# Kernel optimization log

Hardware: AMD Instinct MI355X
Metric: run time of the kernel (lower is better)

## Reference

```python
import jax, jax.numpy as jnp
import numpy as np

N = 100000
IN_C = 256
OUT_C = 256
E = 500000


def gcn_conv(x, W, b, edges):
    """PyG GCNConv: add self-loops, symmetric D^-1/2 (A+I) D^-1/2 normalization,
    then scatter-add of transformed source features into targets, plus bias."""
    n = x.shape[0]
    loop = jnp.arange(n, dtype=edges.dtype)
    row = jnp.concatenate([edges[0], loop])  # source
    col = jnp.concatenate([edges[1], loop])  # target
    deg = jax.ops.segment_sum(jnp.ones_like(col, dtype=x.dtype), col, num_segments=n)
    dis = jax.lax.rsqrt(deg)  # deg >= 1 after self-loops
    norm = dis[row] * dis[col]  # [E+n]
    h = x @ W  # [n, out]
    msg = h[row] * norm[:, None]  # gather + scale
    return jax.ops.segment_sum(msg, col, num_segments=n) + b


def setup_inputs() -> dict:
    key = jax.random.key(0)
    ks = jax.random.split(key, 24)
    x = jax.random.normal(ks[0], (N, IN_C), dtype=jnp.float32)
    edges00 = jax.random.randint(ks[1], (2, E), 0, N, dtype=jnp.int32)
    edges01 = jax.random.randint(ks[2], (2, E), 0, N, dtype=jnp.int32)
    edges10 = jax.random.randint(ks[3], (2, E), 0, N, dtype=jnp.int32)
    edges11 = jax.random.randint(ks[4], (2, E), 0, N, dtype=jnp.int32)
    t0 = (jax.random.uniform(ks[5], (N,)) > 0.5).astype(jnp.float32)
    t1 = 1.0 - t0
    scale = 1.0 / np.sqrt(IN_C)
    W1 = jax.random.normal(ks[6], (IN_C, OUT_C), dtype=jnp.float32) * scale
    W2 = jax.random.normal(ks[7], (IN_C, OUT_C), dtype=jnp.float32) * scale
    W3 = jax.random.normal(ks[8], (IN_C, OUT_C), dtype=jnp.float32) * scale
    W4 = jax.random.normal(ks[9], (IN_C, OUT_C), dtype=jnp.float32) * scale
    b1 = jnp.zeros((OUT_C,), jnp.float32)
    b2 = jnp.zeros((OUT_C,), jnp.float32)
    b3 = jnp.zeros((OUT_C,), jnp.float32)
    b4 = jnp.zeros((OUT_C,), jnp.float32)
    p0 = jax.random.normal(ks[10], (OUT_C,), dtype=jnp.float32)
    p1 = jax.random.normal(ks[11], (OUT_C,), dtype=jnp.float32)
    p2 = jax.random.normal(ks[12], (OUT_C,), dtype=jnp.float32)
    p3 = jax.random.normal(ks[13], (OUT_C,), dtype=jnp.float32)
    p4 = jax.random.normal(ks[14], (OUT_C,), dtype=jnp.float32)
    p5 = jax.random.normal(ks[15], (OUT_C,), dtype=jnp.float32)
    return dict(x=x, edges00=edges00, edges01=edges01, edges10=edges10, edges11=edges11,
                type0_idx=t0, type1_idx=t1,
                W1=W1, b1=b1, W2=W2, b2=b2, W3=W3, b3=b3, W4=W4, b4=b4,
                p0=p0, p1=p1, p2=p2, p3=p3, p4=p4, p5=p5)


def reference(x, edges00, edges01, edges10, edges11, type0_idx, type1_idx,
              W1, b1, W2, b2, W3, b3, W4, b4, p0, p1, p2, p3, p4, p5):
    # x0/x1: first feature column masked by node type, broadcast over out channels
    x0c = type0_idx * x[:, 0]  # [N]
    x1c = type1_idx * x[:, 0]
    x00 = gcn_conv(x, W1, b1, edges00)
    x01 = gcn_conv(x, W2, b2, edges01)
    x10 = gcn_conv(x, W3, b3, edges10)
    x11 = gcn_conv(x, W4, b4, edges11)
    out = (x0c[:, None] * p0 + x1c[:, None] * p1
           + x00 * p2 + x01 * p3 + x10 * p4 + x11 * p5)
    return out
```

## Files before the change

### kernel.cpp

```cpp
#include <hip/hip_runtime.h>


#define PCAP 24

typedef __bf16 v8bf __attribute__((ext_vector_type(8)));
typedef float v4f __attribute__((ext_vector_type(4)));

__device__ __forceinline__ unsigned short f2bf(float f) {
  unsigned u = __float_as_uint(f);
  u += 0x7fffu + ((u >> 16) & 1u);
  return (unsigned short)(u >> 16);
}
__device__ __forceinline__ float bf2f(unsigned short s) {
  return __uint_as_float(((unsigned)s) << 16);
}
__device__ __forceinline__ void async_ld16(const void* g, void* l) {
  __builtin_amdgcn_global_load_lds((__attribute__((address_space(1))) void*)g,
                                   (__attribute__((address_space(3))) void*)l,
                                   16, 0, 0);
}

__global__ void lc_fill(const int* __restrict__ e0, const int* __restrict__ e1,
                        const int* __restrict__ e2, const int* __restrict__ e3,
                        int* __restrict__ cursor, unsigned* __restrict__ payload,
                        int N, int E) {
  int e = blockIdx.x * 256 + threadIdx.x;
  if (e >= E) return;
  int k = blockIdx.y;
  const int* ed = (k == 0) ? e0 : (k == 1) ? e1 : (k == 2) ? e2 : e3;
  int src = ed[e], col = ed[E + e];
  int idx = k * N + col;
  int pos = atomicAdd(&cursor[idx], 1);
  if (pos < PCAP) payload[(size_t)idx * PCAP + pos] = (unsigned)src;
}

__global__ void lc_pack(unsigned* __restrict__ payload, const int* __restrict__ deg,
                        int N) {
  int i = blockIdx.x * 256 + threadIdx.x;
  if (i >= N * PCAP) return;
  int k = blockIdx.y;
  int col = i / PCAP, slot = i - col * PCAP;
  int list = k * N + col;
  int cnt = deg[list];
  if (cnt > PCAP) cnt = PCAP;
  if (slot >= cnt) return;
  size_t pidx = (size_t)list * PCAP + slot;
  unsigned src = payload[pidx];
  float ds = rsqrtf((float)(deg[(size_t)k * N + src] + 1));
  unsigned q = (unsigned)(ds * 32767.0f + 0.5f);
  payload[pidx] = (q << 17) | src;
}

__global__ void lc_prep(const float* __restrict__ W1, const float* __restrict__ W2,
                        const float* __restrict__ W3, const float* __restrict__ W4,
                        const float* __restrict__ b1, const float* __restrict__ b2,
                        const float* __restrict__ b3, const float* __restrict__ b4,
                        const float* __restrict__ p2, const float* __restrict__ p3,
                        const float* __restrict__ p4, const float* __restrict__ p5,
                        unsigned short* __restrict__ Wt, float* __restrict__ biasc) {
  __shared__ float tile[256][33];
  int k = blockIdx.y, co0 = blockIdx.x * 32;
  int t = threadIdx.x;
  const float* W = (k == 0) ? W1 : (k == 1) ? W2 : (k == 2) ? W3 : W4;
  const float* p = (k == 0) ? p2 : (k == 1) ? p3 : (k == 2) ? p4 : p5;

  if (blockIdx.x == 0 && k == 0) {
    int c = t;
    biasc[c] = b1[c] * p2[c] + b2[c] * p3[c] + b3[c] * p4[c] + b4[c] * p5[c];
  }

  int coL = t & 31, kkB = t >> 5;
#pragma unroll 4
  for (int pass = 0; pass < 32; ++pass) {
    int kk = pass * 8 + kkB;
    tile[kk][coL] = W[kk * 256 + co0 + coL];
  }
  __syncthreads();

  int co = t >> 3, seg0 = t & 7;
  float pv = p[co0 + co];
#pragma unroll
  for (int i = 0; i < 4; ++i) {
    int s = seg0 + 8 * i;
    ushort4 lo, hi;
    int kk = s * 8;
    lo.x = f2bf(tile[kk + 0][co] * pv); lo.y = f2bf(tile[kk + 1][co] * pv);
    lo.z = f2bf(tile[kk + 2][co] * pv); lo.w = f2bf(tile[kk + 3][co] * pv);
    hi.x = f2bf(tile[kk + 4][co] * pv); hi.y = f2bf(tile[kk + 5][co] * pv);
    hi.z = f2bf(tile[kk + 6][co] * pv); hi.w = f2bf(tile[kk + 7][co] * pv);
    unsigned short* dst = Wt + (size_t)(co0 + co) * 1024 + k * 256 + kk;
    *(ushort4*)dst = lo;
    *(ushort4*)(dst + 4) = hi;
  }
}

__global__ void lc_cvt(const float4* __restrict__ x4, ushort4* __restrict__ xb4,
                       const float* __restrict__ t0, const float* __restrict__ t1,
                       float* __restrict__ m0, float* __restrict__ m1, int n4) {
  int i = blockIdx.x * 256 + threadIdx.x;
  if (i >= n4) return;
  float4 v = x4[i];
  ushort4 r;
  r.x = f2bf(v.x); r.y = f2bf(v.y); r.z = f2bf(v.z); r.w = f2bf(v.w);
  xb4[i] = r;
  if ((i & 63) == 0) {
    int n = i >> 6;
    float xc = v.x;
    m0[n] = t0[n] * xc;
    m1[n] = t1[n] * xc;
  }
}

__global__ __launch_bounds__(256) void lc_aggx(
    const unsigned short* __restrict__ xb, unsigned short* __restrict__ Agg,
    int aggw, int kcount, int kbase, const int* __restrict__ deg,
    const unsigned* __restrict__ payload, int N) {
  int t = threadIdx.x;
  int w = t >> 6, lane = t & 63;
  int n, k, koff;
  if (kcount == 4) { n = blockIdx.x; k = w; koff = k * 256; }
  else { n = blockIdx.x * 4 + w; k = kbase; koff = 0; }
  if (n >= N) return;
  int c = lane * 4;
  int idx = k * N + n;

  int degv = deg[idx];
  float dn = rsqrtf((float)(degv + 1));
  float dns = dn * (1.0f / 32767.0f);
  float s = dn * dn;
  ushort4 hv = *(const ushort4*)&xb[(size_t)n * 256 + c];
  float a0 = bf2f(hv.x) * s, a1 = bf2f(hv.y) * s;
  float a2 = bf2f(hv.z) * s, a3 = bf2f(hv.w) * s;

  size_t start = (size_t)idx * PCAP;
  int cnt = (degv > PCAP) ? PCAP : degv;
  int i = 0;
  for (; i + 4 <= cnt; i += 4) {
    unsigned p0v = payload[start + i];
    unsigned p1v = payload[start + i + 1];
    unsigned p2v = payload[start + i + 2];
    unsigned p3v = payload[start + i + 3];
    unsigned s0 = p0v & 0x1FFFFu, s1 = p1v & 0x1FFFFu;
    unsigned s2 = p2v & 0x1FFFFu, s3 = p3v & 0x1FFFFu;
    ushort4 g0 = *(const ushort4*)&xb[(size_t)s0 * 256 + c];
    ushort4 g1 = *(const ushort4*)&xb[(size_t)s1 * 256 + c];
    ushort4 g2 = *(const ushort4*)&xb[(size_t)s2 * 256 + c];
    ushort4 g3 = *(const ushort4*)&xb[(size_t)s3 * 256 + c];
    float n0 = (float)(p0v >> 17) * dns, n1 = (float)(p1v >> 17) * dns;
    float n2 = (float)(p2v >> 17) * dns, n3 = (float)(p3v >> 17) * dns;
    a0 += bf2f(g0.x) * n0 + bf2f(g1.x) * n1 + bf2f(g2.x) * n2 + bf2f(g3.x) * n3;
    a1 += bf2f(g0.y) * n0 + bf2f(g1.y) * n1 + bf2f(g2.y) * n2 + bf2f(g3.y) * n3;
    a2 += bf2f(g0.z) * n0 + bf2f(g1.z) * n1 + bf2f(g2.z) * n2 + bf2f(g3.z) * n3;
    a3 += bf2f(g0.w) * n0 + bf2f(g1.w) * n1 + bf2f(g2.w) * n2 + bf2f(g3.w) * n3;
  }
  for (; i < cnt; i++) {
    unsigned p0v = payload[start + i];
    unsigned s0 = p0v & 0x1FFFFu;
    ushort4 g0 = *(const ushort4*)&xb[(size_t)s0 * 256 + c];
    float n0 = (float)(p0v >> 17) * dns;
    a0 += bf2f(g0.x) * n0;
    a1 += bf2f(g0.y) * n0;
    a2 += bf2f(g0.z) * n0;
    a3 += bf2f(g0.w) * n0;
  }
  ushort4 r;
  r.x = f2bf(a0); r.y = f2bf(a1); r.z = f2bf(a2); r.w = f2bf(a3);
  *(ushort4*)&Agg[(size_t)n * aggw + koff + c] = r;
}

__global__ __launch_bounds__(512) void lc_gemm(
    const unsigned short* __restrict__ A, int strideA,
    const unsigned short* __restrict__ B, int strideB, int K,
    float* __restrict__ out, int Mrows, int addprev, int doepi,
    const float* __restrict__ m0, const float* __restrict__ m1,
    const float* __restrict__ p0, const float* __restrict__ p1,
    const float* __restrict__ biasc) {
  __shared__ alignas(16) unsigned short As[2][128 * 32];
  __shared__ alignas(16) unsigned short Bs[2][256 * 32];
  int t = threadIdx.x;
  int w = t >> 6, lane = t & 63;
  int wm = w & 1, wn = w >> 1;
  int quad = lane >> 4, l16 = lane & 15;
  int row0 = blockIdx.x * 128;

  v4f acc[4][4];
#pragma unroll
  for (int mt = 0; mt < 4; mt++)
#pragma unroll
    for (int nt = 0; nt < 4; nt++) {
      v4f z = {0.f, 0.f, 0.f, 0.f};
      acc[mt][nt] = z;
    }

  const int ra = t >> 2;
  const int e0 = (t & 3) * 8;
  const int sws = (ra & 3) << 3;
  const unsigned swf = (unsigned)((l16 & 3) << 3);

  int growA = row0 + ra;
  if (growA >= Mrows) growA = Mrows - 1;
  const unsigned short* Ap = A + (size_t)growA * strideA + (e0 ^ sws);
  const unsigned short* Bp0 = B + (size_t)ra * strideB + (e0 ^ sws);
  const unsigned short* Bp1 = B + (size_t)(128 + ra) * strideB + (e0 ^ sws);
  const int lA = ra * 32 + e0;
  const int lB0 = ra * 32 + e0, lB1 = (128 + ra) * 32 + e0;

  async_ld16(Ap, &As[0][lA]);
  async_ld16(Bp0, &Bs[0][lB0]);
  async_ld16(Bp1, &Bs[0][lB1]);
  asm volatile("s_waitcnt vmcnt(0)" ::: "memory");
  __builtin_amdgcn_s_barrier();

  int cur = 0;
  for (int kk = 0; kk < K; kk += 32) {
    if (kk + 32 < K) {
      async_ld16(Ap + kk + 32, &As[cur ^ 1][lA]);
      async_ld16(Bp0 + kk + 32, &Bs[cur ^ 1][lB0]);
      async_ld16(Bp1 + kk + 32, &Bs[cur ^ 1][lB1]);
    }

    v8bf af[4], bfr[4];
    unsigned eq = ((unsigned)(quad * 8)) ^ swf;
#pragma unroll
    for (int mt = 0; mt < 4; mt++) {
      int r = wm * 64 + mt * 16 + l16;
      af[mt] = *(const v8bf*)&As[cur][(unsigned)r * 32 + eq];
    }
#pragma unroll
    for (int nt = 0; nt < 4; nt++) {
      int n = wn * 64 + nt * 16 + l16;
      bfr[nt] = *(const v8bf*)&Bs[cur][(unsigned)n * 32 + eq];
    }
#pragma unroll
    for (int mt = 0; mt < 4; mt++)
#pragma unroll
      for (int nt = 0; nt < 4; nt++)
        acc[mt][nt] =
            __builtin_amdgcn_mfma_f32_16x16x32_bf16(af[mt], bfr[nt], acc[mt][nt], 0, 0, 0);

    asm volatile("s_waitcnt vmcnt(0)" ::: "memory");
    __builtin_amdgcn_s_barrier();
    cur ^= 1;
  }

  float pc0[4], pc1[4], bc[4];
#pragma unroll
  for (int nt = 0; nt < 4; nt++) {
    int gcol = wn * 64 + nt * 16 + l16;
    pc0[nt] = doepi ? p0[gcol] : 0.f;
    pc1[nt] = doepi ? p1[gcol] : 0.f;
    bc[nt] = doepi ? biasc[gcol] : 0.f;
  }
#pragma unroll
  for (int mt = 0; mt < 4; mt++)
#pragma unroll
    for (int r = 0; r < 4; r++) {
      int grow = row0 + wm * 64 + mt * 16 + quad * 4 + r;
      if (grow >= Mrows) continue;
      float m0v = 0.f, m1v = 0.f;
      if (doepi) { m0v = m0[grow]; m1v = m1[grow]; }
#pragma unroll
      for (int nt = 0; nt < 4; nt++) {
        int gcol = wn * 64 + nt * 16 + l16;
        size_t o = (size_t)grow * 256 + gcol;
        float v = acc[mt][nt][r];
        if (addprev) v += out[o];
        if (doepi) v += m0v * pc0[nt] + m1v * pc1[nt] + bc[nt];
        out[o] = v;
      }
    }
}

extern "C" void kernel_launch(void* const* d_in, const int* in_sizes, int n_in,
                              void* d_out, int out_size, void* d_ws, size_t ws_size,
                              hipStream_t stream) {
  const float* x = (const float*)d_in[0];
  const int* e00 = (const int*)d_in[1];
  const int* e01 = (const int*)d_in[2];
  const int* e10 = (const int*)d_in[3];
  const int* e11 = (const int*)d_in[4];
  const float* t0 = (const float*)d_in[5];
  const float* t1 = (const float*)d_in[6];
  const float* W1 = (const float*)d_in[7];
  const float* b1 = (const float*)d_in[8];
  const float* W2 = (const float*)d_in[9];
  const float* b2 = (const float*)d_in[10];
  const float* W3 = (const float*)d_in[11];
  const float* b3 = (const float*)d_in[12];
  const float* W4 = (const float*)d_in[13];
  const float* b4 = (const float*)d_in[14];
  const float* p0 = (const float*)d_in[15];
  const float* p1 = (const float*)d_in[16];
  const float* p2 = (const float*)d_in[17];
  const float* p3 = (const float*)d_in[18];
  const float* p4 = (const float*)d_in[19];
  const float* p5 = (const float*)d_in[20];
  float* out = (float*)d_out;

  int N = in_sizes[0] / 256;
  int E = in_sizes[1] / 2;
  int M4 = 4 * N;

  char* wp = (char*)d_ws;
  auto carve = [&](size_t bytes) {
    void* r = (void*)wp;
    wp += (bytes + 255) & ~(size_t)255;
    return r;
  };
  unsigned short* xb = (unsigned short*)carve((size_t)N * 256 * 2);
  unsigned short* Wt = (unsigned short*)carve((size_t)256 * 1024 * 2);
  int* cursor = (int*)carve((size_t)M4 * 4);
  float* biasc = (float*)carve(256 * 4);
  float* m0 = (float*)carve((size_t)N * 4);
  float* m1 = (float*)carve((size_t)N * 4);
  unsigned* payload = (unsigned*)carve((size_t)M4 * PCAP * 4);
  size_t used = (size_t)(wp - (char*)d_ws);
  size_t remain = (ws_size > used) ? ws_size - used : 0;
  bool fat = remain >= (size_t)N * 1024 * 2;
  unsigned short* Agg = (unsigned short*)wp;

  int gE = (E + 255) / 256;
  int gP = (N * PCAP + 255) / 256;

  hipMemsetAsync(cursor, 0, (size_t)M4 * 4, stream);
  lc_fill<<<dim3(gE, 4), 256, 0, stream>>>(e00, e01, e10, e11, cursor, payload, N, E);
  lc_pack<<<dim3(gP, 4), 256, 0, stream>>>(payload, cursor, N);
  lc_prep<<<dim3(8, 4), 256, 0, stream>>>(W1, W2, W3, W4, b1, b2, b3, b4,
                                          p2, p3, p4, p5, Wt, biasc);
  lc_cvt<<<(N * 64 + 255) / 256, 256, 0, stream>>>((const float4*)x, (ushort4*)xb,
                                                   t0, t1, m0, m1, N * 64);

  int gemm_mb = (N + 127) / 128;
  if (fat) {
    lc_aggx<<<N, 256, 0, stream>>>(xb, Agg, 1024, 4, 0, cursor, payload, N);
    lc_gemm<<<gemm_mb, 512, 0, stream>>>(Agg, 1024, Wt, 1024, 1024, out, N,
                                         0, 1, m0, m1, p0, p1, biasc);
  } else {
    for (int k = 0; k < 4; k++) {
      lc_aggx<<<(N + 3) / 4, 256, 0, stream>>>(xb, Agg, 256, 1, k, cursor,
                                               payload, N);
      lc_gemm<<<gemm_mb, 512, 0, stream>>>(Agg, 256, Wt + k * 256, 1024, 256,
                                           out, N, (k > 0) ? 1 : 0,
                                           (k == 3) ? 1 : 0, m0, m1, p0, p1,
                                           biasc);
    }
  }
}
```

Measured before the change: 700.0 us.

## Fuse payload packing into fill via separate degree histogram; aggregate two nodes per wave

Adds a histogram pass that computes in-degrees first, so the fill kernel can write the packed source-and-normalization word directly and the separate pack pass goes away. The aggregation kernel now has each wave process two destination nodes at once, with predicated, clamped gathers that keep more independent loads in flight. This costs an extra pass over the edge lists and extra memset traffic. Nodes with unequal degrees also issue wasted clamped loads up to the larger count.

```diff
diff --git a/kernel.cpp b/kernel.cpp
--- a/kernel.cpp
+++ b/kernel.cpp
@@ -20,10 +20,21 @@
                                    16, 0, 0);
 }
 
+__global__ void lc_hist(const int* __restrict__ e0, const int* __restrict__ e1,
+                        const int* __restrict__ e2, const int* __restrict__ e3,
+                        int* __restrict__ deg, int N, int E) {
+  int e = blockIdx.x * 256 + threadIdx.x;
+  if (e >= E) return;
+  int k = blockIdx.y;
+  const int* ed = (k == 0) ? e0 : (k == 1) ? e1 : (k == 2) ? e2 : e3;
+  int col = ed[E + e];
+  atomicAdd(&deg[k * N + col], 1);
+}
+
 __global__ void lc_fill(const int* __restrict__ e0, const int* __restrict__ e1,
                         const int* __restrict__ e2, const int* __restrict__ e3,
-                        int* __restrict__ cursor, unsigned* __restrict__ payload,
-                        int N, int E) {
+                        const int* __restrict__ deg, int* __restrict__ cursor,
+                        unsigned* __restrict__ payload, int N, int E) {
   int e = blockIdx.x * 256 + threadIdx.x;
   if (e >= E) return;
   int k = blockIdx.y;
@@ -31,24 +42,11 @@
   int src = ed[e], col = ed[E + e];
   int idx = k * N + col;
   int pos = atomicAdd(&cursor[idx], 1);
-  if (pos < PCAP) payload[(size_t)idx * PCAP + pos] = (unsigned)src;
-}
-
-__global__ void lc_pack(unsigned* __restrict__ payload, const int* __restrict__ deg,
-                        int N) {
-  int i = blockIdx.x * 256 + threadIdx.x;
-  if (i >= N * PCAP) return;
-  int k = blockIdx.y;
-  int col = i / PCAP, slot = i - col * PCAP;
-  int list = k * N + col;
-  int cnt = deg[list];
-  if (cnt > PCAP) cnt = PCAP;
-  if (slot >= cnt) return;
-  size_t pidx = (size_t)list * PCAP + slot;
-  unsigned src = payload[pidx];
-  float ds = rsqrtf((float)(deg[(size_t)k * N + src] + 1));
-  unsigned q = (unsigned)(ds * 32767.0f + 0.5f);
-  payload[pidx] = (q << 17) | src;
+  if (pos < PCAP) {
+    float ds = rsqrtf((float)(deg[(size_t)k * N + src] + 1));
+    unsigned q = (unsigned)(ds * 32767.0f + 0.5f);
+    payload[(size_t)idx * PCAP + pos] = (q << 17) | (unsigned)src;
+  }
 }
 
 __global__ void lc_prep(const float* __restrict__ W1, const float* __restrict__ W2,
@@ -111,61 +109,68 @@
   }
 }
 
+#define GATP(BASE, POS, LIM, CNT, DNS, A0, A1, A2, A3)                  \
+  do {                                                                  \
+    int jj = ((POS) < (CNT)) ? (POS) : (LIM);                           \
+    unsigned pv = payload[(BASE) + jj];                                 \
+    unsigned ss = pv & 0x1FFFFu;                                        \
+    ushort4 gg = *(const ushort4*)&xb[(size_t)ss * 256 + c];            \
+    float nn = ((POS) < (CNT)) ? (float)(pv >> 17) * (DNS) : 0.f;       \
+    A0 += bf2f(gg.x) * nn;                                              \
+    A1 += bf2f(gg.y) * nn;                                              \
+    A2 += bf2f(gg.z) * nn;                                              \
+    A3 += bf2f(gg.w) * nn;                                              \
+  } while (0)
+
 __global__ __launch_bounds__(256) void lc_aggx(
     const unsigned short* __restrict__ xb, unsigned short* __restrict__ Agg,
     int aggw, int kcount, int kbase, const int* __restrict__ deg,
     const unsigned* __restrict__ payload, int N) {
   int t = threadIdx.x;
   int w = t >> 6, lane = t & 63;
-  int n, k, koff;
-  if (kcount == 4) { n = blockIdx.x; k = w; koff = k * 256; }
-  else { n = blockIdx.x * 4 + w; k = kbase; koff = 0; }
-  if (n >= N) return;
+  int n0, k, koff;
+  if (kcount == 4) { n0 = blockIdx.x * 2; k = w; koff = k * 256; }
+  else { n0 = blockIdx.x * 8 + w * 2; k = kbase; koff = 0; }
+  if (n0 >= N) return;
   int c = lane * 4;
-  int idx = k * N + n;
-
-  int degv = deg[idx];
-  float dn = rsqrtf((float)(degv + 1));
-  float dns = dn * (1.0f / 32767.0f);
-  float s = dn * dn;
-  ushort4 hv = *(const ushort4*)&xb[(size_t)n * 256 + c];
-  float a0 = bf2f(hv.x) * s, a1 = bf2f(hv.y) * s;
-  float a2 = bf2f(hv.z) * s, a3 = bf2f(hv.w) * s;
-
-  size_t start = (size_t)idx * PCAP;
-  int cnt = (degv > PCAP) ? PCAP : degv;
-  int i = 0;
-  for (; i + 4 <= cnt; i += 4) {
-    unsigned p0v = payload[start + i];
-    unsigned p1v = payload[start + i + 1];
-    unsigned p2v = payload[start + i + 2];
-    unsigned p3v = payload[start + i + 3];
-    unsigned s0 = p0v & 0x1FFFFu, s1 = p1v & 0x1FFFFu;
-    unsigned s2 = p2v & 0x1FFFFu, s3 = p3v & 0x1FFFFu;
-    ushort4 g0 = *(const ushort4*)&xb[(size_t)s0 * 256 + c];
-    ushort4 g1 = *(const ushort4*)&xb[(size_t)s1 * 256 + c];
-    ushort4 g2 = *(const ushort4*)&xb[(size_t)s2 * 256 + c];
-    ushort4 g3 = *(const ushort4*)&xb[(size_t)s3 * 256 + c];
-    float n0 = (float)(p0v >> 17) * dns, n1 = (float)(p1v >> 17) * dns;
-    float n2 = (float)(p2v >> 17) * dns, n3 = (float)(p3v >> 17) * dns;
-    a0 += bf2f(g0.x) * n0 + bf2f(g1.x) * n1 + bf2f(g2.x) * n2 + bf2f(g3.x) * n3;
-    a1 += bf2f(g0.y) * n0 + bf2f(g1.y) * n1 + bf2f(g2.y) * n2 + bf2f(g3.y) * n3;
-    a2 += bf2f(g0.z) * n0 + bf2f(g1.z) * n1 + bf2f(g2.z) * n2 + bf2f(g3.z) * n3;
-    a3 += bf2f(g0.w) * n0 + bf2f(g1.w) * n1 + bf2f(g2.w) * n2 + bf2f(g3.w) * n3;
-  }
-  for (; i < cnt; i++) {
-    unsigned p0v = payload[start + i];
-    unsigned s0 = p0v & 0x1FFFFu;
-    ushort4 g0 = *(const ushort4*)&xb[(size_t)s0 * 256 + c];
-    float n0 = (float)(p0v >> 17) * dns;
-    a0 += bf2f(g0.x) * n0;
-    a1 += bf2f(g0.y) * n0;
-    a2 += bf2f(g0.z) * n0;
-    a3 += bf2f(g0.w) * n0;
-  }
-  ushort4 r;
-  r.x = f2bf(a0); r.y = f2bf(a1); r.z = f2bf(a2); r.w = f2bf(a3);
-  *(ushort4*)&Agg[(size_t)n * aggw + koff + c] = r;
+  int n1 = n0 + 1;
+  int n1c = (n1 < N) ? n1 : N - 1;
+  int idx0 = k * N + n0;
+  int idx1 = k * N + n1c;
+
+  int dg0 = deg[idx0], dg1 = deg[idx1];
+  float dn0 = rsqrtf((float)(dg0 + 1)), dn1 = rsqrtf((float)(dg1 + 1));
+  float dns0 = dn0 * (1.0f / 32767.0f), dns1 = dn1 * (1.0f / 32767.0f);
+  float s0 = dn0 * dn0, s1 = dn1 * dn1;
+  ushort4 h0 = *(const ushort4*)&xb[(size_t)n0 * 256 + c];
+  ushort4 h1 = *(const ushort4*)&xb[(size_t)n1c * 256 + c];
+  float a0 = bf2f(h0.x) * s0, a1 = bf2f(h0.y) * s0;
+  float a2 = bf2f(h0.z) * s0, a3 = bf2f(h0.w) * s0;
+  float u0 = bf2f(h1.x) * s1, u1 = bf2f(h1.y) * s1;
+  float u2 = bf2f(h1.z) * s1, u3 = bf2f(h1.w) * s1;
+
+  size_t st0 = (size_t)idx0 * PCAP, st1 = (size_t)idx1 * PCAP;
+  int cnt0 = (dg0 > PCAP) ? PCAP : dg0;
+  int cnt1 = (dg1 > PCAP) ? PCAP : dg1;
+  int lim0 = (cnt0 > 0) ? cnt0 - 1 : 0;
+  int lim1 = (cnt1 > 0) ? cnt1 - 1 : 0;
+  int cmax = (cnt0 > cnt1) ? cnt0 : cnt1;
+  for (int i = 0; i < cmax; i += 4) {
+    GATP(st0, i + 0, lim0, cnt0, dns0, a0, a1, a2, a3);
+    GATP(st0, i + 1, lim0, cnt0, dns0, a0, a1, a2, a3);
+    GATP(st0, i + 2, lim0, cnt0, dns0, a0, a1, a2, a3);
+    GATP(st0, i + 3, lim0, cnt0, dns0, a0, a1, a2, a3);
+    GATP(st1, i + 0, lim1, cnt1, dns1, u0, u1, u2, u3);
+    GATP(st1, i + 1, lim1, cnt1, dns1, u0, u1, u2, u3);
+    GATP(st1, i + 2, lim1, cnt1, dns1, u0, u1, u2, u3);
+    GATP(st1, i + 3, lim1, cnt1, dns1, u0, u1, u2, u3);
+  }
+
+  ushort4 r0, r1;
+  r0.x = f2bf(a0); r0.y = f2bf(a1); r0.z = f2bf(a2); r0.w = f2bf(a3);
+  r1.x = f2bf(u0); r1.y = f2bf(u1); r1.z = f2bf(u2); r1.w = f2bf(u3);
+  *(ushort4*)&Agg[(size_t)n0 * aggw + koff + c] = r0;
+  if (n1 < N) *(ushort4*)&Agg[(size_t)n1 * aggw + koff + c] = r1;
 }
 
 __global__ __launch_bounds__(512) void lc_gemm(
@@ -309,6 +314,7 @@
   };
   unsigned short* xb = (unsigned short*)carve((size_t)N * 256 * 2);
   unsigned short* Wt = (unsigned short*)carve((size_t)256 * 1024 * 2);
+  int* deg = (int*)carve((size_t)M4 * 4);
   int* cursor = (int*)carve((size_t)M4 * 4);
   float* biasc = (float*)carve(256 * 4);
   float* m0 = (float*)carve((size_t)N * 4);
@@ -320,11 +326,11 @@
   unsigned short* Agg = (unsigned short*)wp;
 
   int gE = (E + 255) / 256;
-  int gP = (N * PCAP + 255) / 256;
-
-  hipMemsetAsync(cursor, 0, (size_t)M4 * 4, stream);
-  lc_fill<<<dim3(gE, 4), 256, 0, stream>>>(e00, e01, e10, e11, cursor, payload, N, E);
-  lc_pack<<<dim3(gP, 4), 256, 0, stream>>>(payload, cursor, N);
+
+  hipMemsetAsync(deg, 0, (size_t)2 * M4 * 4, stream);
+  lc_hist<<<dim3(gE, 4), 256, 0, stream>>>(e00, e01, e10, e11, deg, N, E);
+  lc_fill<<<dim3(gE, 4), 256, 0, stream>>>(e00, e01, e10, e11, deg, cursor,
+                                           payload, N, E);
   lc_prep<<<dim3(8, 4), 256, 0, stream>>>(W1, W2, W3, W4, b1, b2, b3, b4,
                                           p2, p3, p4, p5, Wt, biasc);
   lc_cvt<<<(N * 64 + 255) / 256, 256, 0, stream>>>((const float4*)x, (ushort4*)xb,
@@ -332,13 +338,12 @@
 
   int gemm_mb = (N + 127) / 128;
   if (fat) {
-    lc_aggx<<<N, 256, 0, stream>>>(xb, Agg, 1024, 4, 0, cursor, payload, N);
+    lc_aggx<<<(N + 1) / 2, 256, 0, stream>>>(xb, Agg, 1024, 4, 0, deg, payload, N);
     lc_gemm<<<gemm_mb, 512, 0, stream>>>(Agg, 1024, Wt, 1024, 1024, out, N,
                                          0, 1, m0, m1, p0, p1, biasc);
   } else {
     for (int k = 0; k < 4; k++) {
-      lc_aggx<<<(N + 3) / 4, 256, 0, stream>>>(xb, Agg, 256, 1, k, cursor,
-                                               payload, N);
+      lc_aggx<<<(N + 7) / 8, 256, 0, stream>>>(xb, Agg, 256, 1, k, deg, payload, N);
       lc_gemm<<<gemm_mb, 512, 0, stream>>>(Agg, 256, Wt + k * 256, 1024, 256,
                                            out, N, (k > 0) ? 1 : 0,
                                            (k == 3) ? 1 : 0, m0, m1, p0, p1,
```

Measured after the change: 690.6 us. No clear change (-1.4%).
